# Kernel tuning notes

Measured on AMD Instinct MI355X. Metric: run time of the kernel, lower is better.

## Reference

```python
import jax, jax.numpy as jnp
import numpy as np

VOCAB, HIDDEN, EMB_DIM = 30522, 768, 128
B, QLEN, DLEN = 1024, 32, 180
NEG = -1e4  # masked doc-token similarity
EPS = 1e-12


def setup_inputs() -> dict:
    key = jax.random.key(0)
    k1, k2, k3, k4, k5, k6 = jax.random.split(key, 6)
    return {
        "query_input_ids": jax.random.randint(k1, (B, QLEN), 0, VOCAB, dtype=jnp.int64) if jax.config.jax_enable_x64 else jax.random.randint(k1, (B, QLEN), 0, VOCAB, dtype=jnp.int32),
        "query_attention_mask": jax.random.randint(k2, (B, QLEN), 0, 2, dtype=jnp.int32),
        "doc_input_ids": jax.random.randint(k3, (B, DLEN), 0, VOCAB, dtype=jnp.int32),
        "doc_attention_mask": jax.random.randint(k4, (B, DLEN), 0, 2, dtype=jnp.int32),
        "embed_table": jax.random.normal(k5, (VOCAB, HIDDEN), dtype=jnp.float32) * 0.02,
        "proj_w": jax.random.normal(k6, (HIDDEN, EMB_DIM), dtype=jnp.float32) * 0.02,
        "proj_b": jnp.zeros((EMB_DIM,), dtype=jnp.float32),
    }


def _encode(ids, embed_table, proj_w, proj_b):
    # token embedding lookup -> linear projection -> L2 normalize (ColBERT-style)
    h = embed_table[ids]                      # (B, L, HIDDEN)
    e = jnp.einsum('blh,hd->bld', h, proj_w) + proj_b  # (B, L, EMB_DIM)
    e = e / (jnp.linalg.norm(e, axis=-1, keepdims=True) + EPS)
    return e


def reference(query_input_ids, query_attention_mask, doc_input_ids,
              doc_attention_mask, embed_table, proj_w, proj_b):
    q = _encode(query_input_ids, embed_table, proj_w, proj_b)  # (B, Q, D)
    d = _encode(doc_input_ids, embed_table, proj_w, proj_b)    # (B, T, D)
    # Batched MaxSim: sim[b,q,t] = <q_emb, d_emb>
    sim = jnp.einsum('bqd,btd->bqt', q, d)
    sim = jnp.where(doc_attention_mask[:, None, :] > 0, sim, NEG)
    max_sim = sim.max(axis=-1)                                  # (B, Q)
    scores = (max_sim * query_attention_mask.astype(max_sim.dtype)).sum(axis=-1)
    return scores  # (B,)
```

## Files before the change

kernel.cpp:

```cpp
#include <hip/hip_runtime.h>
#include <math.h>

#define VOCAB  30522
#define HIDDEN 768
#define EMB    128
#define BATCH  1024
#define QLEN   32
#define DLEN   180
#define NEGV   (-1e4f)

typedef __attribute__((ext_vector_type(8))) short bf16x8;
typedef __attribute__((ext_vector_type(4))) float f32x4;

__device__ __forceinline__ unsigned short f2bf(float x) {
  union { float f; unsigned u; } v; v.f = x;
  unsigned r = v.u + 0x7FFFu + ((v.u >> 16) & 1u);
  return (unsigned short)(r >> 16);
}
__device__ __forceinline__ float bf2f(unsigned short h) {
  union { float f; unsigned u; } v; v.u = ((unsigned)h) << 16;
  return v.f;
}
__device__ __forceinline__ void split_pk(float x0, float x1, unsigned& h, unsigned& l) {
  asm("v_cvt_pk_bf16_f32 %0, %1, %2" : "=v"(h) : "v"(x0), "v"(x1));
  float h0, h1;
  h0 = __uint_as_float(h << 16);
  h1 = __uint_as_float(h & 0xffff0000u);
  float l0 = x0 - h0, l1 = x1 - h1;
  asm("v_cvt_pk_bf16_f32 %0, %1, %2" : "=v"(l) : "v"(l0), "v"(l1));
}

__global__ __launch_bounds__(256) void prep_wfrag(
    const float* __restrict__ W, unsigned short* __restrict__ wfh,
    unsigned short* __restrict__ wfl) {
  int g = blockIdx.x * 256 + threadIdx.x;
  if (g >= 24 * 8 * 64) return;
  int lane = g & 63, nt = (g >> 6) & 7, kk = g >> 9;
  int lr = lane & 15, kq = lane >> 4;
  int n = nt * 16 + lr;
  int k0 = kk * 32 + kq * 8;
  unsigned short hh[8], ll[8];
#pragma unroll
  for (int j = 0; j < 8; ++j) {
    float x = W[(size_t)(k0 + j) * EMB + n];
    unsigned short hi = f2bf(x);
    hh[j] = hi;
    ll[j] = f2bf(x - bf2f(hi));
  }
  size_t base = (size_t)g * 8;
#pragma unroll
  for (int j = 0; j < 2; ++j) {
    *(ushort4*)(wfh + base + j * 4) = *(ushort4*)(hh + j * 4);
    *(ushort4*)(wfl + base + j * 4) = *(ushort4*)(ll + j * 4);
  }
}

__global__ __launch_bounds__(256) void colbert_proj_mfma(
    const float* __restrict__ emb, const unsigned short* __restrict__ wfh,
    const unsigned short* __restrict__ wfl, const float* __restrict__ bias,
    unsigned short* __restrict__ pebf) {
  __shared__ __align__(16) char smem[32768];

  const int tid  = threadIdx.x;
  const int lane = tid & 63;
  const int wid  = tid >> 6;
  const int lr   = lane & 15;
  const int kq   = lane >> 4;
  const int row0 = blockIdx.x * 32;

  f32x4 acc[2][2];
#pragma unroll
  for (int mi = 0; mi < 2; ++mi)
#pragma unroll
    for (int ni = 0; ni < 2; ++ni) acc[mi][ni] = (f32x4)0.f;

  float4 ar[4];
#pragma unroll
  for (int i = 0; i < 4; ++i) {
    int idx = i * 256 + tid;
    int row = idx >> 5, c4 = idx & 31;
    int gr = row0 + row; if (gr > VOCAB - 1) gr = VOCAB - 1;
    ar[i] = *(const float4*)(emb + (size_t)gr * HIDDEN + c4 * 4);
  }

#define WRITE_A(bufidx)                                                        \
  {                                                                            \
    char* Ahb = smem + (bufidx) * 16384;                                       \
    char* Alb = Ahb + 8192;                                                    \
    _Pragma("unroll")                                                          \
    for (int i = 0; i < 4; ++i) {                                              \
      int idx = i * 256 + tid;                                                 \
      int row = idx >> 5, c4 = idx & 31;                                       \
      unsigned h0, l0, h1, l1;                                                 \
      split_pk(ar[i].x, ar[i].y, h0, l0);                                      \
      split_pk(ar[i].z, ar[i].w, h1, l1);                                      \
      int byt = (row * 256 + c4 * 8) ^ ((row & 7) << 4);                       \
      *(uint2*)(Ahb + byt) = make_uint2(h0, h1);                               \
      *(uint2*)(Alb + byt) = make_uint2(l0, l1);                               \
    }                                                                          \
  }

  WRITE_A(0);
  __syncthreads();

  for (int hc = 0; hc < 6; ++hc) {
    const int cur = hc & 1;
    bf16x8 bh[4][2], bl[4][2];
#pragma unroll
    for (int kk = 0; kk < 4; ++kk)
#pragma unroll
      for (int ni = 0; ni < 2; ++ni) {
        size_t g = ((size_t)((hc * 4 + kk) * 8 + wid * 2 + ni) * 64 + lane) * 8;
        bh[kk][ni] = *(const bf16x8*)(wfh + g);
        bl[kk][ni] = *(const bf16x8*)(wfl + g);
      }
    __builtin_amdgcn_sched_barrier(0);
    if (hc < 5) {
#pragma unroll
      for (int i = 0; i < 4; ++i) {
        int idx = i * 256 + tid;
        int row = idx >> 5, c4 = idx & 31;
        int gr = row0 + row; if (gr > VOCAB - 1) gr = VOCAB - 1;
        ar[i] = *(const float4*)(emb + (size_t)gr * HIDDEN + (hc + 1) * 128 + c4 * 4);
      }
    }
    char* Ahb = smem + cur * 16384;
    char* Alb = Ahb + 8192;
#pragma unroll
    for (int kk = 0; kk < 4; ++kk) {
      bf16x8 ah[2], al[2];
#pragma unroll
      for (int mi = 0; mi < 2; ++mi) {
        int row = mi * 16 + lr;
        int byt = (row * 256 + kk * 64 + kq * 16) ^ ((row & 7) << 4);
        ah[mi] = *(bf16x8*)(Ahb + byt);
        al[mi] = *(bf16x8*)(Alb + byt);
      }
#pragma unroll
      for (int mi = 0; mi < 2; ++mi)
#pragma unroll
        for (int ni = 0; ni < 2; ++ni) {
          acc[mi][ni] = __builtin_amdgcn_mfma_f32_16x16x32_bf16(ah[mi], bh[kk][ni], acc[mi][ni], 0, 0, 0);
          acc[mi][ni] = __builtin_amdgcn_mfma_f32_16x16x32_bf16(ah[mi], bl[kk][ni], acc[mi][ni], 0, 0, 0);
          acc[mi][ni] = __builtin_amdgcn_mfma_f32_16x16x32_bf16(al[mi], bh[kk][ni], acc[mi][ni], 0, 0, 0);
        }
    }
    if (hc < 5) WRITE_A(cur ^ 1);
    __syncthreads();
  }

  float* ep = (float*)smem;
#pragma unroll
  for (int ni = 0; ni < 2; ++ni) {
    int col = wid * 32 + ni * 16 + lr;
    float bb = bias[col];
#pragma unroll
    for (int mi = 0; mi < 2; ++mi)
#pragma unroll
      for (int j = 0; j < 4; ++j) {
        int r = mi * 16 + kq * 4 + j;
        ep[r * 132 + col] = acc[mi][ni][j] + bb;
      }
  }
  __syncthreads();
  {
    int row = tid >> 3, oct = tid & 7;
    float4 vv[4];
    float ss = 0.f;
#pragma unroll
    for (int i = 0; i < 4; ++i) {
      vv[i] = *(float4*)&ep[row * 132 + oct * 16 + i * 4];
      ss += vv[i].x * vv[i].x + vv[i].y * vv[i].y + vv[i].z * vv[i].z + vv[i].w * vv[i].w;
    }
    ss += __shfl_xor(ss, 1);
    ss += __shfl_xor(ss, 2);
    ss += __shfl_xor(ss, 4);
    float sc = 1.f / (sqrtf(ss) + 1e-12f);
    int gr = row0 + row;
    if (gr < VOCAB) {
      unsigned pk[8];
#pragma unroll
      for (int i = 0; i < 4; ++i) {
        pk[i * 2 + 0] = (unsigned)f2bf(vv[i].x * sc) | ((unsigned)f2bf(vv[i].y * sc) << 16);
        pk[i * 2 + 1] = (unsigned)f2bf(vv[i].z * sc) | ((unsigned)f2bf(vv[i].w * sc) << 16);
      }
      uint4* dst = (uint4*)(pebf + (size_t)gr * EMB + oct * 16);
      dst[0] = make_uint4(pk[0], pk[1], pk[2], pk[3]);
      dst[1] = make_uint4(pk[4], pk[5], pk[6], pk[7]);
    }
  }
}

__global__ __launch_bounds__(256) void colbert_score_mfma(
    const int* __restrict__ qids, const int* __restrict__ qmask,
    const int* __restrict__ dids, const int* __restrict__ dmask,
    const unsigned short* __restrict__ pebf, float* __restrict__ out) {
  __shared__ int sqid[32];
  __shared__ int sdid[192];
  __shared__ unsigned char smsk[192];
  __shared__ float wmax[4][32];

  const int b    = blockIdx.x;
  const int tid  = threadIdx.x;
  const int lane = tid & 63;
  const int wid  = tid >> 6;
  const int lr   = lane & 15;
  const int kq   = lane >> 4;

  if (tid < 32) sqid[tid] = qids[b * QLEN + tid];
  if (tid < 192) {
    if (tid < DLEN) {
      sdid[tid] = dids[b * DLEN + tid];
      smsk[tid] = (unsigned char)(dmask[b * DLEN + tid] > 0 ? 1 : 0);
    } else {
      sdid[tid] = 0;
      smsk[tid] = 0;
    }
  }
  __syncthreads();

  bf16x8 af[2][4];
#pragma unroll
  for (int mi = 0; mi < 2; ++mi) {
    size_t base = (size_t)sqid[mi * 16 + lr] * EMB + kq * 8;
#pragma unroll
    for (int ks = 0; ks < 4; ++ks)
      af[mi][ks] = *(const bf16x8*)(pebf + base + ks * 32);
  }
  const int n0 = wid * 48;
  bf16x8 bfr[3][4];
#pragma unroll
  for (int ni = 0; ni < 3; ++ni) {
    size_t base = (size_t)sdid[n0 + ni * 16 + lr] * EMB + kq * 8;
#pragma unroll
    for (int ks = 0; ks < 4; ++ks)
      bfr[ni][ks] = *(const bf16x8*)(pebf + base + ks * 32);
  }

  f32x4 acc[2][3];
#pragma unroll
  for (int mi = 0; mi < 2; ++mi)
#pragma unroll
    for (int ni = 0; ni < 3; ++ni) acc[mi][ni] = (f32x4)0.f;

#pragma unroll
  for (int ks = 0; ks < 4; ++ks)
#pragma unroll
    for (int mi = 0; mi < 2; ++mi)
#pragma unroll
      for (int ni = 0; ni < 3; ++ni)
        acc[mi][ni] = __builtin_amdgcn_mfma_f32_16x16x32_bf16(af[mi][ks], bfr[ni][ks], acc[mi][ni], 0, 0, 0);

#pragma unroll
  for (int mi = 0; mi < 2; ++mi) {
#pragma unroll
    for (int j = 0; j < 4; ++j) {
      float m = -3.0e38f;
#pragma unroll
      for (int ni = 0; ni < 3; ++ni) {
        int t = n0 + ni * 16 + lr;
        float s = smsk[t] ? acc[mi][ni][j] : NEGV;
        m = fmaxf(m, s);
      }
#pragma unroll
      for (int x = 1; x < 16; x <<= 1) m = fmaxf(m, __shfl_xor(m, x));
      if (lr == 0) wmax[wid][mi * 16 + kq * 4 + j] = m;
    }
  }
  __syncthreads();

  if (tid < 32) {
    float m = fmaxf(fmaxf(wmax[0][tid], wmax[1][tid]),
                    fmaxf(wmax[2][tid], wmax[3][tid]));
    float s = m * (float)qmask[b * QLEN + tid];
#pragma unroll
    for (int x = 1; x < 32; x <<= 1) s += __shfl_xor(s, x);
    if (tid == 0) out[b] = s;
  }
}

extern "C" void kernel_launch(void* const* d_in, const int* in_sizes, int n_in,
                              void* d_out, int out_size, void* d_ws, size_t ws_size,
                              hipStream_t stream) {
  const int*   qids  = (const int*)d_in[0];
  const int*   qmask = (const int*)d_in[1];
  const int*   dids  = (const int*)d_in[2];
  const int*   dmask = (const int*)d_in[3];
  const float* emb   = (const float*)d_in[4];
  const float* W     = (const float*)d_in[5];
  const float* bias  = (const float*)d_in[6];
  float*       out   = (float*)d_out;

  char* ws = (char*)d_ws;
  unsigned short* pebf = (unsigned short*)ws;
  unsigned short* wfh  = (unsigned short*)(ws + 7813632);
  unsigned short* wfl  = (unsigned short*)(ws + 7813632 + 196608);

  prep_wfrag<<<48, 256, 0, stream>>>(W, wfh, wfl);
  colbert_proj_mfma<<<(VOCAB + 31) / 32, 256, 0, stream>>>(emb, wfh, wfl, bias, pebf);
  colbert_score_mfma<<<BATCH, 256, 0, stream>>>(qids, qmask, dids, dmask, pebf, out);
}
```

Baseline: 49.75 us.

## Stream fp32 embedding tiles via direct global-to-LDS loads and split at fragment read

The projection kernel now copies raw fp32 embedding rows straight into LDS using global_load_lds, with the XOR swizzle applied on the source address, instead of staging them through registers and writing bf16 hi/lo pairs. The bf16 hi/lo split moves to the point where each wave reads its MFMA fragment, and the K chunk is halved to 64 so the double buffer shrinks to about 17KB. The aim is to cut register pressure and LDS footprint, which could raise occupancy and overlap loads with MFMA work. The cost is redundant split work per fragment read and twice as many loop iterations and barriers.

```diff
diff --git a/kernel.cpp b/kernel.cpp
--- a/kernel.cpp
+++ b/kernel.cpp
@@ -11,6 +11,7 @@
 
 typedef __attribute__((ext_vector_type(8))) short bf16x8;
 typedef __attribute__((ext_vector_type(4))) float f32x4;
+typedef unsigned int u32;
 
 __device__ __forceinline__ unsigned short f2bf(float x) {
   union { float f; unsigned u; } v; v.f = x;
@@ -28,6 +29,11 @@
   h1 = __uint_as_float(h & 0xffff0000u);
   float l0 = x0 - h0, l1 = x1 - h1;
   asm("v_cvt_pk_bf16_f32 %0, %1, %2" : "=v"(l) : "v"(l0), "v"(l1));
+}
+__device__ __forceinline__ void gload16(const float* g, void* l) {
+  __builtin_amdgcn_global_load_lds(
+      (const __attribute__((address_space(1))) u32*)g,
+      (__attribute__((address_space(3))) u32*)l, 16, 0, 0);
 }
 
 __global__ __launch_bounds__(256) void prep_wfrag(
@@ -59,7 +65,7 @@
     const float* __restrict__ emb, const unsigned short* __restrict__ wfh,
     const unsigned short* __restrict__ wfl, const float* __restrict__ bias,
     unsigned short* __restrict__ pebf) {
-  __shared__ __align__(16) char smem[32768];
+  __shared__ __align__(16) char smem[17408];
 
   const int tid  = threadIdx.x;
   const int lane = tid & 63;
@@ -68,73 +74,55 @@
   const int kq   = lane >> 4;
   const int row0 = blockIdx.x * 32;
 
+#define GSRC(P, HC)                                                            \
+  (emb + (size_t)(row0 + ((P) >> 4) > VOCAB - 1 ? VOCAB - 1                    \
+                                                : row0 + ((P) >> 4)) * HIDDEN  \
+       + (HC) * 64 + (((P) & 15) ^ (((P) >> 4) & 7)) * 4)
+
+#define GLOAD(HC, BUF)                                                         \
+  {                                                                            \
+    char* d = smem + (BUF) * 8192;                                             \
+    gload16(GSRC(tid, HC),       d + tid * 16);                                \
+    gload16(GSRC(tid + 256, HC), d + 4096 + tid * 16);                         \
+  }
+
   f32x4 acc[2][2];
 #pragma unroll
   for (int mi = 0; mi < 2; ++mi)
 #pragma unroll
     for (int ni = 0; ni < 2; ++ni) acc[mi][ni] = (f32x4)0.f;
 
-  float4 ar[4];
-#pragma unroll
-  for (int i = 0; i < 4; ++i) {
-    int idx = i * 256 + tid;
-    int row = idx >> 5, c4 = idx & 31;
-    int gr = row0 + row; if (gr > VOCAB - 1) gr = VOCAB - 1;
-    ar[i] = *(const float4*)(emb + (size_t)gr * HIDDEN + c4 * 4);
-  }
-
-#define WRITE_A(bufidx)                                                        \
-  {                                                                            \
-    char* Ahb = smem + (bufidx) * 16384;                                       \
-    char* Alb = Ahb + 8192;                                                    \
-    _Pragma("unroll")                                                          \
-    for (int i = 0; i < 4; ++i) {                                              \
-      int idx = i * 256 + tid;                                                 \
-      int row = idx >> 5, c4 = idx & 31;                                       \
-      unsigned h0, l0, h1, l1;                                                 \
-      split_pk(ar[i].x, ar[i].y, h0, l0);                                      \
-      split_pk(ar[i].z, ar[i].w, h1, l1);                                      \
-      int byt = (row * 256 + c4 * 8) ^ ((row & 7) << 4);                       \
-      *(uint2*)(Ahb + byt) = make_uint2(h0, h1);                               \
-      *(uint2*)(Alb + byt) = make_uint2(l0, l1);                               \
-    }                                                                          \
-  }
-
-  WRITE_A(0);
-  __syncthreads();
-
-  for (int hc = 0; hc < 6; ++hc) {
+  GLOAD(0, 0);
+  __syncthreads();
+
+  for (int hc = 0; hc < 12; ++hc) {
     const int cur = hc & 1;
-    bf16x8 bh[4][2], bl[4][2];
-#pragma unroll
-    for (int kk = 0; kk < 4; ++kk)
+    if (hc < 11) GLOAD(hc + 1, cur ^ 1);
+    bf16x8 bh[2][2], bl[2][2];
+#pragma unroll
+    for (int kk = 0; kk < 2; ++kk)
 #pragma unroll
       for (int ni = 0; ni < 2; ++ni) {
-        size_t g = ((size_t)((hc * 4 + kk) * 8 + wid * 2 + ni) * 64 + lane) * 8;
+        size_t g = ((size_t)((hc * 2 + kk) * 8 + wid * 2 + ni) * 64 + lane) * 8;
         bh[kk][ni] = *(const bf16x8*)(wfh + g);
         bl[kk][ni] = *(const bf16x8*)(wfl + g);
       }
-    __builtin_amdgcn_sched_barrier(0);
-    if (hc < 5) {
-#pragma unroll
-      for (int i = 0; i < 4; ++i) {
-        int idx = i * 256 + tid;
-        int row = idx >> 5, c4 = idx & 31;
-        int gr = row0 + row; if (gr > VOCAB - 1) gr = VOCAB - 1;
-        ar[i] = *(const float4*)(emb + (size_t)gr * HIDDEN + (hc + 1) * 128 + c4 * 4);
-      }
-    }
-    char* Ahb = smem + cur * 16384;
-    char* Alb = Ahb + 8192;
-#pragma unroll
-    for (int kk = 0; kk < 4; ++kk) {
+    char* Ab = smem + cur * 8192;
+#pragma unroll
+    for (int kk = 0; kk < 2; ++kk) {
       bf16x8 ah[2], al[2];
 #pragma unroll
       for (int mi = 0; mi < 2; ++mi) {
         int row = mi * 16 + lr;
-        int byt = (row * 256 + kk * 64 + kq * 16) ^ ((row & 7) << 4);
-        ah[mi] = *(bf16x8*)(Ahb + byt);
-        al[mi] = *(bf16x8*)(Alb + byt);
+        int base = row * 256 + kk * 128 + kq * 32;
+        float4 x0 = *(float4*)(Ab + ((base)      ^ ((row & 7) << 4)));
+        float4 x1 = *(float4*)(Ab + ((base + 16) ^ ((row & 7) << 4)));
+        union { unsigned u[4]; bf16x8 v; } H, L;
+        split_pk(x0.x, x0.y, H.u[0], L.u[0]);
+        split_pk(x0.z, x0.w, H.u[1], L.u[1]);
+        split_pk(x1.x, x1.y, H.u[2], L.u[2]);
+        split_pk(x1.z, x1.w, H.u[3], L.u[3]);
+        ah[mi] = H.v; al[mi] = L.v;
       }
 #pragma unroll
       for (int mi = 0; mi < 2; ++mi)
@@ -145,7 +133,6 @@
           acc[mi][ni] = __builtin_amdgcn_mfma_f32_16x16x32_bf16(al[mi], bh[kk][ni], acc[mi][ni], 0, 0, 0);
         }
     }
-    if (hc < 5) WRITE_A(cur ^ 1);
     __syncthreads();
   }
 
@@ -189,6 +176,8 @@
       dst[1] = make_uint4(pk[4], pk[5], pk[6], pk[7]);
     }
   }
+#undef GSRC
+#undef GLOAD
 }
 
 __global__ __launch_bounds__(256) void colbert_score_mfma(
```

After: 51.94 us. 4.4% more time.
